# Kernel optimization log

Measured on AMD Instinct MI355X. Metric: run time of the kernel, lower is better.

The kernel has to match this reference:

```python
import jax, jax.numpy as jnp
import numpy as np

B, T, D, R = 4, 2048, 1024, 32


def setup_inputs() -> dict:
    key = jax.random.key(0)
    kx, ku = jax.random.split(key)
    x = jax.random.normal(kx, (B, T, D), dtype=jnp.float32)
    # low-rank metric factor; small init so distances are moderate
    U = jax.random.normal(ku, (D, R), dtype=jnp.float32) * 0.05
    return {"x": x, "U": U}


def reference(x, U):
    # g = U @ U.T (PSD low-rank metric).
    # dist_sq[b,t,j] = (x_t - x_j)^T g (x_t - x_j)
    #               = ||U^T x_t||^2 + ||U^T x_j||^2 - 2 (U^T x_t).(U^T x_j)
    # Algebraic expansion of the original O(B*T*T*D) broadcasted diff tensor.
    y = jnp.einsum('btd,dr->btr', x, U)                # [B,T,R]
    n = jnp.sum(y * y, axis=-1)                         # [B,T]
    cross = jnp.einsum('btr,bjr->btj', y, y)            # [B,T,T]
    dist_sq = n[:, :, None] + n[:, None, :] - 2.0 * cross
    attn = jax.nn.softmax(-dist_sq, axis=-1)            # [B,T,T]
    return jnp.einsum('btj,bjd->btd', attn, x)          # [B,T,D]
```

## Files before the change

kernel.cpp:

```cpp
#include <hip/hip_runtime.h>
#include <hip/hip_bf16.h>

#define B_ 4
#define T_ 2048
#define D_ 1024
#define R_ 32
#define XP 136

typedef __attribute__((ext_vector_type(8))) short short8;
typedef __attribute__((ext_vector_type(4))) float f32x4;
typedef __attribute__((ext_vector_type(4))) unsigned short us4;
typedef __attribute__((ext_vector_type(8))) unsigned short us8;

__device__ __forceinline__ unsigned short f2bf(float f) {
  union { float f; unsigned u; } v; v.f = f;
  unsigned r = (v.u + 0x7fffu + ((v.u >> 16) & 1u)) >> 16;
  return (unsigned short)r;
}
__device__ __forceinline__ float bf2f(unsigned short h) {
  union { unsigned u; float f; } v; v.u = (unsigned)h << 16;
  return v.f;
}
__device__ __forceinline__ unsigned pk2bf(float a, float b) {
  union { __hip_bfloat162 h; unsigned u; } v;
  v.h = __float22bfloat162_rn(make_float2(a, b));
  return v.u;
}

__global__ __launch_bounds__(256)
void geo_prep(const float* __restrict__ x, const float* __restrict__ U,
              unsigned short* __restrict__ xt, float* __restrict__ ypart) {
  __shared__ unsigned short xs[128 * XP];
  __shared__ unsigned short uts[32 * XP];
  const int bb = blockIdx.y, t0 = blockIdx.x * 128, d0 = blockIdx.z * 128;
  const int tid = threadIdx.x, w = tid >> 6, lane = tid & 63;
  const int m = lane & 15, quad = lane >> 4;

  f32x4 uv[4];
  #pragma unroll
  for (int p = 0; p < 4; p++) {
    const int i4 = p * 256 + tid;
    uv[p] = *(const f32x4*)(U + (size_t)(d0 + (i4 >> 3)) * R_ + (i4 & 7) * 4);
  }
  f32x4 xv[16];
  #pragma unroll
  for (int p = 0; p < 16; p++) {
    const int i4 = p * 256 + tid;
    xv[p] = *(const f32x4*)(x + ((size_t)bb * T_ + t0 + (i4 >> 5)) * D_ + d0 + (i4 & 31) * 4);
  }
  #pragma unroll
  for (int p = 0; p < 4; p++) {
    const int i4 = p * 256 + tid; const int du = i4 >> 3, ru4 = i4 & 7;
    #pragma unroll
    for (int k = 0; k < 4; k++) uts[(ru4 * 4 + k) * XP + du] = f2bf(uv[p][k]);
  }
  #pragma unroll
  for (int p = 0; p < 16; p++) {
    const int i4 = p * 256 + tid; const int r = i4 >> 5, c4 = i4 & 31;
    union { us4 c; unsigned u[2]; } cc;
    cc.u[0] = pk2bf(xv[p][0], xv[p][1]);
    cc.u[1] = pk2bf(xv[p][2], xv[p][3]);
    *(us4*)&xs[r * XP + ((c4 >> 1) ^ (r & 7)) * 8 + (c4 & 1) * 4] = cc.c;
  }
  __syncthreads();
  {
    const int ts = tid & 15, dsb = tid >> 4;
    us8 rowv[8];
    #pragma unroll
    for (int k = 0; k < 8; k++)
      rowv[k] = *(const us8*)&xs[(ts * 8 + k) * XP + ((dsb ^ k) * 8)];
    unsigned short* xo = xt + ((size_t)bb * D_ + d0 + dsb * 8) * T_ + t0 + ts * 8;
    #pragma unroll
    for (int dd = 0; dd < 8; dd++) {
      us8 o;
      #pragma unroll
      for (int k = 0; k < 8; k++) o[k] = rowv[k][dd];
      *(us8*)(xo + (size_t)dd * T_) = o;
    }
  }
  f32x4 acc[2][2];
  #pragma unroll
  for (int i = 0; i < 2; i++)
    #pragma unroll
    for (int j = 0; j < 2; j++) acc[i][j] = (f32x4){0.f, 0.f, 0.f, 0.f};
  #pragma unroll
  for (int ks = 0; ks < 4; ks++) {
    const int ko = ks * 32 + quad * 8;
    const int go = ((ks * 4 + quad) ^ (m & 7)) * 8;
    short8 a0 = *(const short8*)&xs[(w * 32 + m) * XP + go];
    short8 a1 = *(const short8*)&xs[(w * 32 + 16 + m) * XP + go];
    short8 b0 = *(const short8*)&uts[m * XP + ko];
    short8 b1 = *(const short8*)&uts[(16 + m) * XP + ko];
    acc[0][0] = __builtin_amdgcn_mfma_f32_16x16x32_bf16(a0, b0, acc[0][0], 0, 0, 0);
    acc[0][1] = __builtin_amdgcn_mfma_f32_16x16x32_bf16(a0, b1, acc[0][1], 0, 0, 0);
    acc[1][0] = __builtin_amdgcn_mfma_f32_16x16x32_bf16(a1, b0, acc[1][0], 0, 0, 0);
    acc[1][1] = __builtin_amdgcn_mfma_f32_16x16x32_bf16(a1, b1, acc[1][1], 0, 0, 0);
  }
  #pragma unroll
  for (int tb = 0; tb < 2; tb++)
    #pragma unroll
    for (int nb = 0; nb < 2; nb++)
      *(f32x4*)(ypart + ((size_t)(blockIdx.z * B_ + bb) * R_ + nb * 16 + m) * T_
                + t0 + w * 32 + tb * 16 + quad * 4) = acc[tb][nb];
}

__global__ __launch_bounds__(256)
void geo_reduce(const float* __restrict__ ypart, unsigned short* __restrict__ ybf,
                float* __restrict__ nsq) {
  __shared__ float ls[32][36];
  const int t0 = blockIdx.x * 32, bb = blockIdx.y;
  const int tid = threadIdx.x;
  {
    const int r = tid >> 3, t4 = (tid & 7) * 4;
    f32x4 v = {0.f, 0.f, 0.f, 0.f};
    #pragma unroll
    for (int s = 0; s < 8; s++) {
      f32x4 p = *(const f32x4*)(ypart + ((size_t)(s * B_ + bb) * R_ + r) * T_ + t0 + t4);
      #pragma unroll
      for (int k = 0; k < 4; k++) v[k] += p[k];
    }
    *(f32x4*)&ls[r][t4] = v;
  }
  __syncthreads();
  const int t = tid >> 3, r4 = (tid & 7) * 4;
  us4 pk; float part = 0.f;
  #pragma unroll
  for (int k = 0; k < 4; k++) {
    const unsigned short h = f2bf(1.69864446f * ls[r4 + k][t]);
    const float bv = bf2f(h); part += bv * bv; pk[k] = h;
  }
  *(us4*)(ybf + ((size_t)bb * T_ + t0 + t) * R_ + r4) = pk;
  part += __shfl_xor(part, 1, 64);
  part += __shfl_xor(part, 2, 64);
  part += __shfl_xor(part, 4, 64);
  if ((tid & 7) == 0) nsq[bb * T_ + t0 + t] = 0.5f * part;
}

__global__ __launch_bounds__(256, 4)
void geo_fused(const unsigned short* __restrict__ ybf,
               const float* __restrict__ nsq,
               const unsigned short* __restrict__ xt,
               float* __restrict__ out) {
  __shared__ unsigned short Bs[2][128 * 64];
  __shared__ float l_s[64];
  const int bz = blockIdx.z, id = blockIdx.x;
  const int d0 = (id & 7) * 128;
  const int t0 = (id >> 3) * 64;
  const int tid = threadIdx.x, w = tid >> 6, lane = tid & 63;
  const int m = lane & 15, quad = lane >> 4;
  const int srow = lane >> 3, sslot = lane & 7;
  const int th = w & 1, dh = w >> 1;

  const unsigned short* yb = ybf + (size_t)bz * T_ * R_;
  const float* nq = nsq + bz * T_;
  const unsigned short* Xb = xt + ((size_t)bz * D_ + d0) * T_;

#define STAGE(J0, BUF) do {                                                      \
    _Pragma("unroll")                                                            \
    for (int cc = 0; cc < 4; cc++) {                                             \
      const int rbase = w * 32 + cc * 8;                                         \
      const int row = rbase + srow;                                              \
      const int sw = (sslot ^ (row & 7)) * 8;                                    \
      __builtin_amdgcn_global_load_lds(                                          \
        (const __attribute__((address_space(1))) void*)(Xb + (size_t)row * T_ + (J0) + sw), \
        (__attribute__((address_space(3))) void*)(&Bs[BUF][rbase * 64]), 16, 0, 0); \
    } } while (0)

  short8 at[2]; float nnt[2]; f32x4 lsum4[2];
  #pragma unroll
  for (int tb = 0; tb < 2; tb++) {
    at[tb] = *(const short8*)(yb + (size_t)(t0 + th * 32 + tb * 16 + m) * R_ + quad * 8);
    nnt[tb] = -nq[t0 + th * 32 + tb * 16 + m];
    lsum4[tb] = (f32x4){0.f, 0.f, 0.f, 0.f};
  }

  f32x4 acc[2][4];
  #pragma unroll
  for (int i = 0; i < 2; i++)
    #pragma unroll
    for (int j = 0; j < 4; j++) acc[i][j] = (f32x4){0.f, 0.f, 0.f, 0.f};

  STAGE(0, 0);

  for (int it = 0; it < 32; ++it) {
    const int j0 = it * 64, buf = it & 1;
    short8 aj[4]; f32x4 njv[4];
    #pragma unroll
    for (int ja = 0; ja < 4; ja++) {
      const int jr = 32 * (ja >> 1) + 8 * (m >> 2) + (ja & 1) * 4 + (m & 3);
      aj[ja] = *(const short8*)(yb + (size_t)(j0 + jr) * R_ + quad * 8);
      njv[ja] = *(const f32x4*)(nq + j0 + 32 * (ja >> 1) + (ja & 1) * 4 + 8 * quad);
    }
    union { short8 s; unsigned u[4]; } pf[2][2];
    #pragma unroll
    for (int tb = 0; tb < 2; tb++) {
      #pragma unroll
      for (int ja = 0; ja < 4; ja++) {
        f32x4 cin;
        #pragma unroll
        for (int r = 0; r < 4; r++) cin[r] = nnt[tb] - njv[ja][r];
        f32x4 c = __builtin_amdgcn_mfma_f32_16x16x32_bf16(aj[ja], at[tb], cin, 0, 0, 0);
        f32x4 p;
        #pragma unroll
        for (int r = 0; r < 4; r++) {
          p[r] = __builtin_amdgcn_exp2f(c[r]);
          lsum4[tb][r] += p[r];
        }
        pf[tb][ja >> 1].u[(ja & 1) * 2 + 0] = pk2bf(p[0], p[1]);
        pf[tb][ja >> 1].u[(ja & 1) * 2 + 1] = pk2bf(p[2], p[3]);
      }
    }
    __syncthreads();
    if (it + 1 < 32) STAGE(j0 + 64, buf ^ 1);
    #pragma unroll
    for (int kb = 0; kb < 2; kb++) {
      short8 bfr[4];
      #pragma unroll
      for (int nb = 0; nb < 4; nb++)
        bfr[nb] = *(const short8*)&Bs[buf][(dh * 64 + nb * 16 + m) * 64 + (((kb * 4 + quad) ^ (m & 7)) * 8)];
      #pragma unroll
      for (int tb = 0; tb < 2; tb++)
        #pragma unroll
        for (int nb = 0; nb < 4; nb++)
          acc[tb][nb] = __builtin_amdgcn_mfma_f32_16x16x32_bf16(pf[tb][kb].s, bfr[nb], acc[tb][nb], 0, 0, 0);
    }
  }
  #pragma unroll
  for (int tb = 0; tb < 2; tb++) {
    float lsum = lsum4[tb][0] + lsum4[tb][1] + lsum4[tb][2] + lsum4[tb][3];
    lsum += __shfl_xor(lsum, 16, 64);
    lsum += __shfl_xor(lsum, 32, 64);
    if (quad == 0 && dh == 0) l_s[th * 32 + tb * 16 + m] = lsum;
  }
  __syncthreads();
  #pragma unroll
  for (int tb = 0; tb < 2; tb++) {
    f32x4 lv = *(const f32x4*)&l_s[th * 32 + tb * 16 + quad * 4];
    f32x4 inv;
    #pragma unroll
    for (int r = 0; r < 4; r++) inv[r] = 1.f / lv[r];
    float* ob = out + ((size_t)bz * T_ + t0 + th * 32 + tb * 16 + quad * 4) * D_ + d0 + dh * 64;
    #pragma unroll
    for (int nb = 0; nb < 4; nb++)
      #pragma unroll
      for (int r = 0; r < 4; r++)
        ob[(size_t)r * D_ + nb * 16 + m] = acc[tb][nb][r] * inv[r];
  }
#undef STAGE
}

extern "C" void kernel_launch(void* const* d_in, const int* in_sizes, int n_in,
                              void* d_out, int out_size, void* d_ws, size_t ws_size,
                              hipStream_t stream) {
  const float* x = (const float*)d_in[0];
  const float* U = (const float*)d_in[1];
  float* out = (float*)d_out;

  const size_t xt_b  = (size_t)B_ * D_ * T_ * 2;
  const size_t ybf_b = (size_t)B_ * T_ * R_ * 2;
  const size_t nsq_b = (size_t)B_ * T_ * 4;
  const size_t yp_b  = (size_t)8 * B_ * R_ * T_ * 4;

  char* wp = (char*)d_ws;
  unsigned short* xtp = (unsigned short*)wp;                 wp += xt_b;
  unsigned short* ybf = (unsigned short*)wp;                 wp += ybf_b;
  float* nsq = (float*)wp;                                   wp += nsq_b;
  float* ypart = (float*)wp;                                 wp += yp_b;
  (void)ws_size; (void)in_sizes; (void)n_in; (void)out_size;

  hipLaunchKernelGGL(geo_prep, dim3(T_ / 128, B_, D_ / 128), dim3(256), 0, stream,
                     x, U, xtp, ypart);
  hipLaunchKernelGGL(geo_reduce, dim3(T_ / 32, B_), dim3(256), 0, stream,
                     ypart, ybf, nsq);
  hipLaunchKernelGGL(geo_fused, dim3((T_ / 64) * (D_ / 128), 1, B_), dim3(256), 0, stream,
                     ybf, nsq, xtp, out);
}
```

Before: 168.9 us.

## Share softmax probabilities across warps via LDS and enlarge the query tile

The query tile per block grows from 64 to 128 rows. Each warp now computes exp scores for a disjoint 32 rows and writes them as bf16 into a padded, swizzled LDS tile, so the duplicated score/exp work between the d-halves goes away. The PV matmul then uses a 2x2 warp layout that reuses both the P tile and the X tile from LDS, and the next key block's y/norm values are prefetched into registers. In exchange the X tile is single-buffered with an extra barrier per step, P takes an LDS round trip, launch bounds drop to 2 blocks per CU, and the grid is half as large.

```diff
diff --git a/kernel.cpp b/kernel.cpp
--- a/kernel.cpp
+++ b/kernel.cpp
@@ -6,6 +6,7 @@
 #define D_ 1024
 #define R_ 32
 #define XP 136
+#define ASTR 136
 
 typedef __attribute__((ext_vector_type(8))) short short8;
 typedef __attribute__((ext_vector_type(4))) float f32x4;
@@ -136,26 +137,28 @@
   if ((tid & 7) == 0) nsq[bb * T_ + t0 + t] = 0.5f * part;
 }
 
-__global__ __launch_bounds__(256, 4)
+__global__ __launch_bounds__(256, 2)
 void geo_fused(const unsigned short* __restrict__ ybf,
                const float* __restrict__ nsq,
                const unsigned short* __restrict__ xt,
                float* __restrict__ out) {
-  __shared__ unsigned short Bs[2][128 * 64];
-  __shared__ float l_s[64];
+  __shared__ unsigned short As[128 * (ASTR / 2)];
+  __shared__ unsigned short Bs[128 * 64];
+  __shared__ float l_s[128];
   const int bz = blockIdx.z, id = blockIdx.x;
   const int d0 = (id & 7) * 128;
-  const int t0 = (id >> 3) * 64;
+  const int t0 = (id >> 3) * 128;
   const int tid = threadIdx.x, w = tid >> 6, lane = tid & 63;
   const int m = lane & 15, quad = lane >> 4;
+  const int wr = (w & 1) * 64, wc = (w >> 1) * 64;
   const int srow = lane >> 3, sslot = lane & 7;
-  const int th = w & 1, dh = w >> 1;
+  const int tw = w * 32;
 
   const unsigned short* yb = ybf + (size_t)bz * T_ * R_;
   const float* nq = nsq + bz * T_;
   const unsigned short* Xb = xt + ((size_t)bz * D_ + d0) * T_;
 
-#define STAGE(J0, BUF) do {                                                      \
+#define STAGE(J0) do {                                                           \
     _Pragma("unroll")                                                            \
     for (int cc = 0; cc < 4; cc++) {                                             \
       const int rbase = w * 32 + cc * 8;                                         \
@@ -163,66 +166,81 @@
       const int sw = (sslot ^ (row & 7)) * 8;                                    \
       __builtin_amdgcn_global_load_lds(                                          \
         (const __attribute__((address_space(1))) void*)(Xb + (size_t)row * T_ + (J0) + sw), \
-        (__attribute__((address_space(3))) void*)(&Bs[BUF][rbase * 64]), 16, 0, 0); \
+        (__attribute__((address_space(3))) void*)(Bs + rbase * 64), 16, 0, 0);   \
     } } while (0)
 
   short8 at[2]; float nnt[2]; f32x4 lsum4[2];
   #pragma unroll
   for (int tb = 0; tb < 2; tb++) {
-    at[tb] = *(const short8*)(yb + (size_t)(t0 + th * 32 + tb * 16 + m) * R_ + quad * 8);
-    nnt[tb] = -nq[t0 + th * 32 + tb * 16 + m];
+    at[tb] = *(const short8*)(yb + (size_t)(t0 + tw + tb * 16 + m) * R_ + quad * 8);
+    nnt[tb] = -nq[t0 + tw + tb * 16 + m];
     lsum4[tb] = (f32x4){0.f, 0.f, 0.f, 0.f};
   }
 
-  f32x4 acc[2][4];
-  #pragma unroll
-  for (int i = 0; i < 2; i++)
+  f32x4 acc[4][4];
+  #pragma unroll
+  for (int i = 0; i < 4; i++)
     #pragma unroll
     for (int j = 0; j < 4; j++) acc[i][j] = (f32x4){0.f, 0.f, 0.f, 0.f};
 
-  STAGE(0, 0);
-
-  for (int it = 0; it < 32; ++it) {
-    const int j0 = it * 64, buf = it & 1;
-    short8 aj[4]; f32x4 njv[4];
+  short8 aj[4]; f32x4 njv[4];
+  #pragma unroll
+  for (int ja = 0; ja < 4; ja++) {
+    aj[ja] = *(const short8*)(yb + (size_t)(ja * 16 + m) * R_ + quad * 8);
+    njv[ja] = *(const f32x4*)(nq + ja * 16 + quad * 4);
+  }
+
+  for (int j0 = 0; j0 < T_; j0 += 64) {
+    __syncthreads();
+    STAGE(j0);
+    short8 caj[4]; f32x4 cnj[4];
+    #pragma unroll
+    for (int ja = 0; ja < 4; ja++) { caj[ja] = aj[ja]; cnj[ja] = njv[ja]; }
+    const int jn = (j0 + 64 < T_) ? j0 + 64 : 0;
     #pragma unroll
     for (int ja = 0; ja < 4; ja++) {
-      const int jr = 32 * (ja >> 1) + 8 * (m >> 2) + (ja & 1) * 4 + (m & 3);
-      aj[ja] = *(const short8*)(yb + (size_t)(j0 + jr) * R_ + quad * 8);
-      njv[ja] = *(const f32x4*)(nq + j0 + 32 * (ja >> 1) + (ja & 1) * 4 + 8 * quad);
-    }
-    union { short8 s; unsigned u[4]; } pf[2][2];
+      aj[ja] = *(const short8*)(yb + (size_t)(jn + ja * 16 + m) * R_ + quad * 8);
+      njv[ja] = *(const f32x4*)(nq + jn + ja * 16 + quad * 4);
+    }
     #pragma unroll
     for (int tb = 0; tb < 2; tb++) {
+      const int trow = tw + tb * 16 + m;
       #pragma unroll
       for (int ja = 0; ja < 4; ja++) {
         f32x4 cin;
         #pragma unroll
-        for (int r = 0; r < 4; r++) cin[r] = nnt[tb] - njv[ja][r];
-        f32x4 c = __builtin_amdgcn_mfma_f32_16x16x32_bf16(aj[ja], at[tb], cin, 0, 0, 0);
+        for (int r = 0; r < 4; r++) cin[r] = nnt[tb] - cnj[ja][r];
+        f32x4 c = __builtin_amdgcn_mfma_f32_16x16x32_bf16(caj[ja], at[tb], cin, 0, 0, 0);
+        union { us4 c; unsigned u[2]; } pk;
         f32x4 p;
         #pragma unroll
         for (int r = 0; r < 4; r++) {
           p[r] = __builtin_amdgcn_exp2f(c[r]);
           lsum4[tb][r] += p[r];
         }
-        pf[tb][ja >> 1].u[(ja & 1) * 2 + 0] = pk2bf(p[0], p[1]);
-        pf[tb][ja >> 1].u[(ja & 1) * 2 + 1] = pk2bf(p[2], p[3]);
+        pk.u[0] = pk2bf(p[0], p[1]);
+        pk.u[1] = pk2bf(p[2], p[3]);
+        const int sb = ja * 2 + (quad >> 1);
+        char* dst = (char*)As + trow * ASTR + ((sb ^ (trow & 7)) * 16) + (quad & 1) * 8;
+        *(us4*)dst = pk.c;
       }
     }
     __syncthreads();
-    if (it + 1 < 32) STAGE(j0 + 64, buf ^ 1);
-    #pragma unroll
-    for (int kb = 0; kb < 2; kb++) {
-      short8 bfr[4];
-      #pragma unroll
-      for (int nb = 0; nb < 4; nb++)
-        bfr[nb] = *(const short8*)&Bs[buf][(dh * 64 + nb * 16 + m) * 64 + (((kb * 4 + quad) ^ (m & 7)) * 8)];
-      #pragma unroll
-      for (int tb = 0; tb < 2; tb++)
+    #pragma unroll
+    for (int ks = 0; ks < 2; ks++) {
+      short8 af[4], bf[4];
+      #pragma unroll
+      for (int i = 0; i < 4; i++) {
+        const int ra = wr + i * 16 + m;
+        af[i] = *(const short8*)((const char*)As + ra * ASTR + (((ks * 4 + quad) ^ (m & 7)) * 16));
+        const int cd = wc + i * 16 + m;
+        bf[i] = *(const short8*)&Bs[cd * 64 + (((ks * 4 + quad) ^ (m & 7)) * 8)];
+      }
+      #pragma unroll
+      for (int rb = 0; rb < 4; rb++)
         #pragma unroll
-        for (int nb = 0; nb < 4; nb++)
-          acc[tb][nb] = __builtin_amdgcn_mfma_f32_16x16x32_bf16(pf[tb][kb].s, bfr[nb], acc[tb][nb], 0, 0, 0);
+        for (int cb = 0; cb < 4; cb++)
+          acc[rb][cb] = __builtin_amdgcn_mfma_f32_16x16x32_bf16(af[rb], bf[cb], acc[rb][cb], 0, 0, 0);
     }
   }
   #pragma unroll
@@ -230,21 +248,21 @@
     float lsum = lsum4[tb][0] + lsum4[tb][1] + lsum4[tb][2] + lsum4[tb][3];
     lsum += __shfl_xor(lsum, 16, 64);
     lsum += __shfl_xor(lsum, 32, 64);
-    if (quad == 0 && dh == 0) l_s[th * 32 + tb * 16 + m] = lsum;
+    if (quad == 0) l_s[tw + tb * 16 + m] = lsum;
   }
   __syncthreads();
   #pragma unroll
-  for (int tb = 0; tb < 2; tb++) {
-    f32x4 lv = *(const f32x4*)&l_s[th * 32 + tb * 16 + quad * 4];
+  for (int rb = 0; rb < 4; rb++) {
+    f32x4 lv = *(const f32x4*)&l_s[wr + rb * 16 + quad * 4];
     f32x4 inv;
     #pragma unroll
     for (int r = 0; r < 4; r++) inv[r] = 1.f / lv[r];
-    float* ob = out + ((size_t)bz * T_ + t0 + th * 32 + tb * 16 + quad * 4) * D_ + d0 + dh * 64;
-    #pragma unroll
-    for (int nb = 0; nb < 4; nb++)
+    float* ob = out + ((size_t)bz * T_ + t0 + wr + rb * 16 + quad * 4) * D_ + d0 + wc;
+    #pragma unroll
+    for (int cb = 0; cb < 4; cb++)
       #pragma unroll
       for (int r = 0; r < 4; r++)
-        ob[(size_t)r * D_ + nb * 16 + m] = acc[tb][nb][r] * inv[r];
+        ob[(size_t)r * D_ + cb * 16 + m] = acc[rb][cb][r] * inv[r];
   }
 #undef STAGE
 }
@@ -272,6 +290,6 @@
                      x, U, xtp, ypart);
   hipLaunchKernelGGL(geo_reduce, dim3(T_ / 32, B_), dim3(256), 0, stream,
                      ypart, ybf, nsq);
-  hipLaunchKernelGGL(geo_fused, dim3((T_ / 64) * (D_ / 128), 1, B_), dim3(256), 0, stream,
+  hipLaunchKernelGGL(geo_fused, dim3((T_ / 128) * (D_ / 128), 1, B_), dim3(256), 0, stream,
                      ybf, nsq, xtp, out);
 }
```

Measured after the change: 149.1 us. 1.13x faster.
